# Performance work log

Hardware: AMD Instinct MI355X
Metric: run time of the kernel (lower is better)

The kernel has to match this reference:

```python
import jax, jax.numpy as jnp
import numpy as np
import math

D_MODEL = 1024
N_HEADS = 16
D_HEAD = 64
D_MLP = 4096
INIT_RANGE = 0.02
VAR_EPS = 1e-05
BATCH = 2
SEQ = 2048


def new_gelu(x):
    c = math.sqrt(2.0 / math.pi)
    return 0.5 * x * (1.0 + jnp.tanh(c * (x + 0.044715 * x ** 3)))


def layer_norm(x, w, b):
    mean = jnp.mean(x, axis=-1, keepdims=True)
    x = x - mean
    var = jnp.mean(x * x, axis=-1, keepdims=True)
    return x / jnp.sqrt(var + VAR_EPS) * w + b


def setup_inputs() -> dict:
    key = jax.random.key(0)
    ks = jax.random.split(key, 12)
    s = INIT_RANGE
    return {
        "resid": jax.random.normal(ks[0], (BATCH, SEQ, D_MODEL), jnp.float32),
        "w_q": s * jax.random.normal(ks[1], (N_HEADS, D_MODEL, D_HEAD), jnp.float32),
        "w_k": s * jax.random.normal(ks[2], (N_HEADS, D_MODEL, D_HEAD), jnp.float32),
        "w_v": s * jax.random.normal(ks[3], (N_HEADS, D_MODEL, D_HEAD), jnp.float32),
        "w_o": s * jax.random.normal(ks[4], (N_HEADS, D_HEAD, D_MODEL), jnp.float32),
        "ln1_w": s * jax.random.normal(ks[5], (D_MODEL,), jnp.float32),
        "ln1_b": jnp.zeros((D_MODEL,), jnp.float32),
        "ln2_w": s * jax.random.normal(ks[6], (D_MODEL,), jnp.float32),
        "ln2_b": jnp.zeros((D_MODEL,), jnp.float32),
        "w_in": s * jax.random.normal(ks[7], (D_MODEL, D_MLP), jnp.float32),
        "b_in": jnp.zeros((D_MLP,), jnp.float32),
        "w_out": s * jax.random.normal(ks[8], (D_MLP, D_MODEL), jnp.float32),
        "b_out": jnp.zeros((D_MODEL,), jnp.float32),
    }


def attention(x, w_q, w_k, w_v, w_o):
    # x: [b, s, d]; weights: [h, d, dh] / [h, dh, d]
    qs = jnp.einsum('bsd,hde->bhse', x, w_q)
    ks = jnp.einsum('bsd,hde->bhse', x, w_k)
    vs = jnp.einsum('bsd,hde->bhse', x, w_v)
    attn = jnp.einsum('bhqe,bhke->bhqk', qs, ks)  # [b, h, s, s]
    s = attn.shape[-1]
    causal = jnp.triu(jnp.ones((s, s), dtype=bool), k=1)
    attn = jnp.where(causal, -jnp.inf, attn)
    attn = jax.nn.softmax(attn / math.sqrt(D_HEAD), axis=-1)
    z = jnp.einsum('bhqk,bhke->bhqe', attn, vs)
    return jnp.einsum('bhse,hed->bsd', z, w_o)


def reference(resid, w_q, w_k, w_v, w_o, ln1_w, ln1_b, ln2_w, ln2_b, w_in, b_in, w_out, b_out):
    resid = resid + attention(layer_norm(resid, ln1_w, ln1_b), w_q, w_k, w_v, w_o)
    h = layer_norm(resid, ln2_w, ln2_b)
    h = new_gelu(jnp.einsum('bsd,dm->bsm', h, w_in) + b_in)
    resid = resid + jnp.einsum('bsm,md->bsd', h, w_out) + b_out
    return resid
```

## Files before the change

### kernel.cpp

```cpp
#include <hip/hip_runtime.h>

#define DEV static __device__ __forceinline__

typedef unsigned short u16;
typedef __attribute__((ext_vector_type(8))) __bf16 bf16x8;
typedef __attribute__((ext_vector_type(4))) float f32x4;

DEV float bf2f(u16 u) { union { unsigned int i; float f; } v; v.i = ((unsigned int)u) << 16; return v.f; }
DEV u16 f2bf(float f) {
  union { float f; unsigned int i; } v; v.f = f;
  unsigned int r = v.i + 0x7fffu + ((v.i >> 16) & 1u);
  return (u16)(r >> 16);
}

DEV float gelu_f(float x) {
  float u = 0.7978845608028654f * (x + 0.044715f * x * x * x);
  float e = __expf(2.f * u);
  float t = 1.f - 2.f / (e + 1.f);
  return 0.5f * x * (1.f + t);
}

DEV void async16(const u16* g, u16* l) {
  __builtin_amdgcn_global_load_lds(
      (const __attribute__((address_space(1))) unsigned int*)g,
      (__attribute__((address_space(3))) unsigned int*)l, 16, 0, 0);
}

__global__ __launch_bounds__(256) void transpose_all(
    const float* __restrict__ w_q, const float* __restrict__ w_k,
    const float* __restrict__ w_v, const float* __restrict__ w_o,
    const float* __restrict__ w_in, const float* __restrict__ w_out,
    u16* __restrict__ WQKVT, u16* __restrict__ WOT,
    u16* __restrict__ WINT, u16* __restrict__ WOUTT)
{
  int t = blockIdx.x;
  const float* src; u16* dst; int R, C, c0, r0;
  if (t < 3072) {
    int seg = t >> 10, tt = t & 1023;
    int z = tt >> 6, rem = tt & 63;
    const float* w = seg == 0 ? w_q : (seg == 1 ? w_k : w_v);
    src = w + z * 65536;
    dst = WQKVT + seg * 1048576 + z * 65536;
    R = 1024; C = 64;
    c0 = (rem >> 5) * 32; r0 = (rem & 31) * 32;
  } else if (t < 4096) {
    int tt = t - 3072;
    src = w_o; dst = WOT; R = 1024; C = 1024;
    c0 = (tt & 31) * 32; r0 = (tt >> 5) * 32;
  } else if (t < 8192) {
    int tt = t - 4096;
    src = w_in; dst = WINT; R = 1024; C = 4096;
    c0 = (tt & 127) * 32; r0 = (tt >> 7) * 32;
  } else {
    int tt = t - 8192;
    src = w_out; dst = WOUTT; R = 4096; C = 1024;
    c0 = (tt & 31) * 32; r0 = (tt >> 5) * 32;
  }
  __shared__ float tile[32][33];
  int tx = threadIdx.x & 31, ty = threadIdx.x >> 5;
#pragma unroll
  for (int i = 0; i < 32; i += 8)
    tile[ty + i][tx] = src[(size_t)(r0 + ty + i) * C + (c0 + tx)];
  __syncthreads();
#pragma unroll
  for (int i = 0; i < 32; i += 8)
    dst[(size_t)(c0 + ty + i) * R + (r0 + tx)] = f2bf(tile[tx][ty + i]);
}

__global__ __launch_bounds__(256) void ln_kernel(
    const float* __restrict__ x, const float* __restrict__ g,
    const float* __restrict__ b, u16* __restrict__ out)
{
  int row = blockIdx.x, tid = threadIdx.x;
  const float4 v = ((const float4*)(x + (size_t)row * 1024))[tid];
  float s = v.x + v.y + v.z + v.w;
  float ss = v.x * v.x + v.y * v.y + v.z * v.z + v.w * v.w;
#pragma unroll
  for (int m = 1; m < 64; m <<= 1) { s += __shfl_xor(s, m, 64); ss += __shfl_xor(ss, m, 64); }
  __shared__ float red[8];
  if ((tid & 63) == 0) { red[tid >> 6] = s; red[4 + (tid >> 6)] = ss; }
  __syncthreads();
  s = red[0] + red[1] + red[2] + red[3];
  ss = red[4] + red[5] + red[6] + red[7];
  float mean = s * (1.f / 1024.f);
  float var = ss * (1.f / 1024.f) - mean * mean;
  float rstd = rsqrtf(var + 1e-5f);
  float4 gv = ((const float4*)g)[tid];
  float4 bv = ((const float4*)b)[tid];
  u16* o = out + (size_t)row * 1024 + tid * 4;
  o[0] = f2bf((v.x - mean) * rstd * gv.x + bv.x);
  o[1] = f2bf((v.y - mean) * rstd * gv.y + bv.y);
  o[2] = f2bf((v.z - mean) * rstd * gv.z + bv.z);
  o[3] = f2bf((v.w - mean) * rstd * gv.w + bv.w);
}

template <int EPI, int BM, int BN>
__global__ __launch_bounds__(256) void gemm_bf16(
    const u16* __restrict__ A, const u16* __restrict__ Bt, int K, int N,
    const float* __restrict__ addv, const float* __restrict__ bias,
    float* __restrict__ outF, u16* __restrict__ o0, u16* __restrict__ o1,
    u16* __restrict__ o2)
{
  constexpr int IM = BM / 32, IN = BN / 32;
  __shared__ u16 lA[BM * 64];
  __shared__ u16 lB[BN * 64];
  const int tid = threadIdx.x;
  const int lane = tid & 63, wave = tid >> 6;
  const int wm = wave >> 1, wn = wave & 1;
  const int quad = lane >> 4, l16 = lane & 15;
  const int m0 = blockIdx.y * BM, n0 = blockIdx.x * BN;

  f32x4 acc[IM][IN] = {};

  const int srow = lane >> 3;
  const int soff = ((lane & 7) ^ srow) << 3;

  for (int kt = 0; kt < K; kt += 64) {
    __syncthreads();
#pragma unroll
    for (int q = 0; q < BM / 32; ++q) {
      int rbase = wave * (BM / 4) + q * 8;
      async16(A + (size_t)(m0 + rbase + srow) * K + kt + soff, lA + rbase * 64);
    }
#pragma unroll
    for (int q = 0; q < BN / 32; ++q) {
      int rbase = wave * (BN / 4) + q * 8;
      async16(Bt + (size_t)(n0 + rbase + srow) * K + kt + soff, lB + rbase * 64);
    }
    __syncthreads();
#pragma unroll
    for (int kk = 0; kk < 2; ++kk) {
      bf16x8 af[IM], bfr[IN];
#pragma unroll
      for (int i = 0; i < IM; ++i) {
        int ar = wm * (BM / 2) + i * 16 + l16;
        af[i] = *(const bf16x8*)&lA[ar * 64 + ((((kk * 4) + quad) ^ (ar & 7)) << 3)];
      }
#pragma unroll
      for (int j = 0; j < IN; ++j) {
        int br = wn * (BN / 2) + j * 16 + l16;
        bfr[j] = *(const bf16x8*)&lB[br * 64 + ((((kk * 4) + quad) ^ (br & 7)) << 3)];
      }
#pragma unroll
      for (int i = 0; i < IM; ++i)
#pragma unroll
        for (int j = 0; j < IN; ++j)
          acc[i][j] = __builtin_amdgcn_mfma_f32_16x16x32_bf16(af[i], bfr[j], acc[i][j], 0, 0, 0);
    }
  }

#pragma unroll
  for (int i = 0; i < IM; ++i) {
    const int rowb = m0 + wm * (BM / 2) + i * 16 + quad * 4;
#pragma unroll
    for (int j = 0; j < IN; ++j) {
      const int col = n0 + wn * (BN / 2) + j * 16 + l16;
#pragma unroll
      for (int rr = 0; rr < 4; ++rr) {
        const int m = rowb + rr;
        const float v = acc[i][j][rr];
        if (EPI == 0) {
          int bb = m >> 11, s = m & 2047;
          int proj = col >> 10, hc = col & 1023, hh = hc >> 6, e = hc & 63;
          size_t bhh = (size_t)(bb * 16 + hh);
          if (proj == 0) o0[(bhh * 2048 + s) * 64 + e] = f2bf(v * 0.125f);
          else if (proj == 1) o1[(bhh * 2048 + s) * 64 + e] = f2bf(v);
          else o2[bhh * 131072 + (size_t)e * 2048 + s] = f2bf(v);
        } else if (EPI == 1) {
          size_t idx = (size_t)m * N + col;
          outF[idx] = v + addv[idx];
        } else if (EPI == 2) {
          o0[(size_t)m * N + col] = f2bf(gelu_f(v + bias[col]));
        } else {
          size_t idx = (size_t)m * N + col;
          outF[idx] = v + bias[col] + addv[idx];
        }
      }
    }
  }
}

__global__ __launch_bounds__(256) void attn_flash(
    const u16* __restrict__ Q, const u16* __restrict__ K,
    const u16* __restrict__ Vt, u16* __restrict__ Z)
{
  __shared__ u16 lK[64 * 64];
  __shared__ u16 lV[64 * 64];
  __shared__ u16 lP[4][16 * 64];

  const int tid = threadIdx.x;
  const int lane = tid & 63, wave = tid >> 6;
  const int quad = lane >> 4, l16 = lane & 15;

  const int flat = blockIdx.x;
  const int xcd = flat & 7, w = flat >> 3;
  const int bhid = xcd * 4 + (w >> 5);
  const int qtile = 31 - (w & 31);
  const int b = bhid >> 4, h = bhid & 15;
  const size_t bh = (size_t)bhid;
  const int q0b = qtile * 64;
  const int q0w = q0b + wave * 16;

  const int srow = lane >> 3;
  const int soff = ((lane & 7) ^ srow) << 3;

  bf16x8 qf[2];
#pragma unroll
  for (int d = 0; d < 2; ++d)
    qf[d] = *(const bf16x8*)(Q + (bh * 2048 + (size_t)(q0w + l16)) * 64 + d * 32 + quad * 8);

  f32x4 oacc[4] = {};
  float lrow[4] = {};

  u16* myP = lP[wave];
  const int kend = q0b + 64;

  for (int kt0 = 0; kt0 < kend; kt0 += 64) {
    __syncthreads();
#pragma unroll
    for (int q = 0; q < 2; ++q) {
      int rbase = wave * 16 + q * 8;
      async16(K + (bh * 2048 + (size_t)(kt0 + rbase + srow)) * 64 + soff, lK + rbase * 64);
      async16(Vt + bh * 131072 + (size_t)(rbase + srow) * 2048 + kt0 + soff, lV + rbase * 64);
    }
    __syncthreads();

    bf16x8 kf[4][2];
#pragma unroll
    for (int j = 0; j < 4; ++j)
#pragma unroll
      for (int d = 0; d < 2; ++d) {
        int key = j * 16 + l16;
        kf[j][d] = *(const bf16x8*)(lK + key * 64 + (((d * 4 + quad) ^ (key & 7)) << 3));
      }
    f32x4 sv[4];
#pragma unroll
    for (int j = 0; j < 4; ++j) {
      f32x4 z = {};
      z = __builtin_amdgcn_mfma_f32_16x16x32_bf16(qf[0], kf[j][0], z, 0, 0, 0);
      z = __builtin_amdgcn_mfma_f32_16x16x32_bf16(qf[1], kf[j][1], z, 0, 0, 0);
      sv[j] = z;
    }

    const bool needMask = (kt0 + 63 > q0w);
#pragma unroll
    for (int rr = 0; rr < 4; ++rr) {
      int rowl = quad * 4 + rr;
      int rowg = q0w + rowl;
      u16* prow = myP + rowl * 64;
      float accl = lrow[rr];
#pragma unroll
      for (int j = 0; j < 4; ++j) {
        float p = __expf(sv[j][rr]);
        if (needMask && (kt0 + j * 16 + l16 > rowg)) p = 0.f;
        accl += p;
        int chk = j * 2 + (l16 >> 3);
        prow[((chk ^ (rowl & 7)) << 3) + (l16 & 7)] = (u16)(__float_as_uint(p) >> 16);
      }
      lrow[rr] = accl;
    }

#pragma unroll
    for (int ks = 0; ks < 2; ++ks) {
      int chk = ks * 4 + quad;
      bf16x8 pf, vf[4];
      pf = *(const bf16x8*)(myP + l16 * 64 + ((chk ^ (l16 & 7)) << 3));
#pragma unroll
      for (int d = 0; d < 4; ++d) {
        int dh = d * 16 + l16;
        vf[d] = *(const bf16x8*)(lV + dh * 64 + ((chk ^ (dh & 7)) << 3));
      }
#pragma unroll
      for (int d = 0; d < 4; ++d)
        oacc[d] = __builtin_amdgcn_mfma_f32_16x16x32_bf16(pf, vf[d], oacc[d], 0, 0, 0);
    }
  }

#pragma unroll
  for (int rr = 0; rr < 4; ++rr) {
    float l = lrow[rr];
#pragma unroll
    for (int msk = 1; msk < 16; msk <<= 1) l += __shfl_xor(l, msk, 64);
    lrow[rr] = 1.f / l;
  }
#pragma unroll
  for (int d = 0; d < 4; ++d)
#pragma unroll
    for (int rr = 0; rr < 4; ++rr) {
      int srowq = q0w + quad * 4 + rr;
      Z[((size_t)(b * 2048 + srowq)) * 1024 + h * 64 + d * 16 + l16] =
          f2bf(oacc[d][rr] * lrow[rr]);
    }
}

extern "C" void kernel_launch(void* const* d_in, const int* in_sizes, int n_in,
                              void* d_out, int out_size, void* d_ws, size_t ws_size,
                              hipStream_t stream) {
  const float* resid = (const float*)d_in[0];
  const float* w_q  = (const float*)d_in[1];
  const float* w_k  = (const float*)d_in[2];
  const float* w_v  = (const float*)d_in[3];
  const float* w_o  = (const float*)d_in[4];
  const float* ln1w = (const float*)d_in[5];
  const float* ln1b = (const float*)d_in[6];
  const float* ln2w = (const float*)d_in[7];
  const float* ln2b = (const float*)d_in[8];
  const float* w_in = (const float*)d_in[9];
  const float* b_in = (const float*)d_in[10];
  const float* w_out= (const float*)d_in[11];
  const float* b_out= (const float*)d_in[12];
  float* out = (float*)d_out;

  const size_t MB = 1u << 20;
  char* ws = (char*)d_ws;
  u16* WQKVT = (u16*)(ws + 0);
  u16* WOT   = (u16*)(ws + 6 * MB);
  u16* WINT  = (u16*)(ws + 8 * MB);
  u16* WOUTT = (u16*)(ws + 16 * MB);
  u16* X1    = (u16*)(ws + 24 * MB);
  u16* Qb    = (u16*)(ws + 32 * MB);
  u16* Kb    = (u16*)(ws + 40 * MB);
  u16* Vb    = (u16*)(ws + 48 * MB);
  u16* Zb    = (u16*)(ws + 56 * MB);
  float* R2  = (float*)(ws + 64 * MB);
  u16* Hb    = (u16*)(ws + 80 * MB);
  u16* Gb    = (u16*)(ws + 24 * MB);

  transpose_all<<<dim3(12288), 256, 0, stream>>>(w_q, w_k, w_v, w_o, w_in, w_out,
                                                 WQKVT, WOT, WINT, WOUTT);
  ln_kernel<<<4096, 256, 0, stream>>>(resid, ln1w, ln1b, X1);
  gemm_bf16<0, 64, 128><<<dim3(24, 64), 256, 0, stream>>>(X1, WQKVT, 1024, 3072, nullptr, nullptr, nullptr, Qb, Kb, Vb);
  attn_flash<<<dim3(1024), 256, 0, stream>>>(Qb, Kb, Vb, Zb);
  gemm_bf16<1, 64, 64><<<dim3(16, 64), 256, 0, stream>>>(Zb, WOT, 1024, 1024, resid, nullptr, R2, nullptr, nullptr, nullptr);
  ln_kernel<<<4096, 256, 0, stream>>>(R2, ln2w, ln2b, Hb);
  gemm_bf16<2, 64, 128><<<dim3(32, 64), 256, 0, stream>>>(Hb, WINT, 1024, 4096, nullptr, b_in, nullptr, Gb, nullptr, nullptr);
  gemm_bf16<3, 64, 64><<<dim3(16, 64), 256, 0, stream>>>(Gb, WOUTT, 4096, 1024, R2, b_out, out, nullptr, nullptr, nullptr);
}
```

Baseline: 368.1 us.

## Pair causal query tiles per block and double-buffer K/V loads in attention

Each attention block now handles two query tiles, one long and one short (p and 31-p), so every block does the same 33 key-tile iterations and causal work is balanced across half as many blocks. K/V tiles are double-buffered in LDS, and the next tile's async load is issued before computing on the current one, which drops one barrier per iteration. The cost is doubled K/V LDS use, which may lower occupancy, and a longer serial loop per block.

```diff
diff --git a/kernel.cpp b/kernel.cpp
--- a/kernel.cpp
+++ b/kernel.cpp
@@ -184,8 +184,8 @@
     const u16* __restrict__ Q, const u16* __restrict__ K,
     const u16* __restrict__ Vt, u16* __restrict__ Z)
 {
-  __shared__ u16 lK[64 * 64];
-  __shared__ u16 lV[64 * 64];
+  __shared__ u16 lK[2][64 * 64];
+  __shared__ u16 lV[2][64 * 64];
   __shared__ u16 lP[4][16 * 64];
 
   const int tid = threadIdx.x;
@@ -194,36 +194,82 @@
 
   const int flat = blockIdx.x;
   const int xcd = flat & 7, w = flat >> 3;
-  const int bhid = xcd * 4 + (w >> 5);
-  const int qtile = 31 - (w & 31);
+  const int bhid = xcd * 4 + (w >> 4);
+  const int p = w & 15;
   const int b = bhid >> 4, h = bhid & 15;
   const size_t bh = (size_t)bhid;
-  const int q0b = qtile * 64;
-  const int q0w = q0b + wave * 16;
+
+  const int nA = 32 - p;
+  const int q0A = (31 - p) * 64;
+  const int q0B = p * 64;
 
   const int srow = lane >> 3;
   const int soff = ((lane & 7) ^ srow) << 3;
 
+  u16* myP = lP[wave];
+
+  auto stage = [&](int buf, int s) {
+    int kt0 = (s < nA ? s : s - nA) * 64;
+#pragma unroll
+    for (int q = 0; q < 2; ++q) {
+      int rbase = wave * 16 + q * 8;
+      async16(K + (bh * 2048 + (size_t)(kt0 + rbase + srow)) * 64 + soff,
+              lK[buf] + rbase * 64);
+      async16(Vt + bh * 131072 + (size_t)(rbase + srow) * 2048 + kt0 + soff,
+              lV[buf] + rbase * 64);
+    }
+  };
+
+  stage(0, 0);
+
+  f32x4 oacc[4] = {};
+  float lrow[4] = {};
+  int q0w = q0A + wave * 16;
+
   bf16x8 qf[2];
 #pragma unroll
   for (int d = 0; d < 2; ++d)
     qf[d] = *(const bf16x8*)(Q + (bh * 2048 + (size_t)(q0w + l16)) * 64 + d * 32 + quad * 8);
 
-  f32x4 oacc[4] = {};
-  float lrow[4] = {};
-
-  u16* myP = lP[wave];
-  const int kend = q0b + 64;
-
-  for (int kt0 = 0; kt0 < kend; kt0 += 64) {
+  auto writeO = [&]() {
+#pragma unroll
+    for (int rr = 0; rr < 4; ++rr) {
+      float l = lrow[rr];
+#pragma unroll
+      for (int msk = 1; msk < 16; msk <<= 1) l += __shfl_xor(l, msk, 64);
+      lrow[rr] = 1.f / l;
+    }
+#pragma unroll
+    for (int d = 0; d < 4; ++d)
+#pragma unroll
+      for (int rr = 0; rr < 4; ++rr) {
+        int srowq = q0w + quad * 4 + rr;
+        Z[((size_t)(b * 2048 + srowq)) * 1024 + h * 64 + d * 16 + l16] =
+            f2bf(oacc[d][rr] * lrow[rr]);
+      }
+  };
+
+  for (int s = 0; s < 33; ++s) {
+    if (s == nA) {
+      writeO();
+#pragma unroll
+      for (int d = 0; d < 4; ++d)
+#pragma unroll
+        for (int e = 0; e < 4; ++e) oacc[d][e] = 0.f;
+#pragma unroll
+      for (int rr = 0; rr < 4; ++rr) lrow[rr] = 0.f;
+      q0w = q0B + wave * 16;
+#pragma unroll
+      for (int d = 0; d < 2; ++d)
+        qf[d] = *(const bf16x8*)(Q + (bh * 2048 + (size_t)(q0w + l16)) * 64 + d * 32 + quad * 8);
+    }
+
     __syncthreads();
-#pragma unroll
-    for (int q = 0; q < 2; ++q) {
-      int rbase = wave * 16 + q * 8;
-      async16(K + (bh * 2048 + (size_t)(kt0 + rbase + srow)) * 64 + soff, lK + rbase * 64);
-      async16(Vt + bh * 131072 + (size_t)(rbase + srow) * 2048 + kt0 + soff, lV + rbase * 64);
-    }
-    __syncthreads();
+    if (s < 32) stage((s + 1) & 1, s + 1);
+
+    const u16* cK = lK[s & 1];
+    const u16* cV = lV[s & 1];
+    const int kt0 = (s < nA ? s : s - nA) * 64;
 
     bf16x8 kf[4][2];
 #pragma unroll
@@ -231,7 +277,7 @@
 #pragma unroll
       for (int d = 0; d < 2; ++d) {
         int key = j * 16 + l16;
-        kf[j][d] = *(const bf16x8*)(lK + key * 64 + (((d * 4 + quad) ^ (key & 7)) << 3));
+        kf[j][d] = *(const bf16x8*)(cK + key * 64 + (((d * 4 + quad) ^ (key & 7)) << 3));
       }
     f32x4 sv[4];
 #pragma unroll
@@ -251,11 +297,11 @@
       float accl = lrow[rr];
 #pragma unroll
       for (int j = 0; j < 4; ++j) {
-        float p = __expf(sv[j][rr]);
-        if (needMask && (kt0 + j * 16 + l16 > rowg)) p = 0.f;
-        accl += p;
+        float pv = __expf(sv[j][rr]);
+        if (needMask && (kt0 + j * 16 + l16 > rowg)) pv = 0.f;
+        accl += pv;
         int chk = j * 2 + (l16 >> 3);
-        prow[((chk ^ (rowl & 7)) << 3) + (l16 & 7)] = (u16)(__float_as_uint(p) >> 16);
+        prow[((chk ^ (rowl & 7)) << 3) + (l16 & 7)] = (u16)(__float_as_uint(pv) >> 16);
       }
       lrow[rr] = accl;
     }
@@ -268,7 +314,7 @@
 #pragma unroll
       for (int d = 0; d < 4; ++d) {
         int dh = d * 16 + l16;
-        vf[d] = *(const bf16x8*)(lV + dh * 64 + ((chk ^ (dh & 7)) << 3));
+        vf[d] = *(const bf16x8*)(cV + dh * 64 + ((chk ^ (dh & 7)) << 3));
       }
 #pragma unroll
       for (int d = 0; d < 4; ++d)
@@ -276,21 +322,7 @@
     }
   }
 
-#pragma unroll
-  for (int rr = 0; rr < 4; ++rr) {
-    float l = lrow[rr];
-#pragma unroll
-    for (int msk = 1; msk < 16; msk <<= 1) l += __shfl_xor(l, msk, 64);
-    lrow[rr] = 1.f / l;
-  }
-#pragma unroll
-  for (int d = 0; d < 4; ++d)
-#pragma unroll
-    for (int rr = 0; rr < 4; ++rr) {
-      int srowq = q0w + quad * 4 + rr;
-      Z[((size_t)(b * 2048 + srowq)) * 1024 + h * 64 + d * 16 + l16] =
-          f2bf(oacc[d][rr] * lrow[rr]);
-    }
+  writeO();
 }
 
 extern "C" void kernel_launch(void* const* d_in, const int* in_sizes, int n_in,
@@ -330,7 +362,7 @@
                                                  WQKVT, WOT, WINT, WOUTT);
   ln_kernel<<<4096, 256, 0, stream>>>(resid, ln1w, ln1b, X1);
   gemm_bf16<0, 64, 128><<<dim3(24, 64), 256, 0, stream>>>(X1, WQKVT, 1024, 3072, nullptr, nullptr, nullptr, Qb, Kb, Vb);
-  attn_flash<<<dim3(1024), 256, 0, stream>>>(Qb, Kb, Vb, Zb);
+  attn_flash<<<dim3(512), 256, 0, stream>>>(Qb, Kb, Vb, Zb);
   gemm_bf16<1, 64, 64><<<dim3(16, 64), 256, 0, stream>>>(Zb, WOT, 1024, 1024, resid, nullptr, R2, nullptr, nullptr, nullptr);
   ln_kernel<<<4096, 256, 0, stream>>>(R2, ln2w, ln2b, Hb);
   gemm_bf16<2, 64, 128><<<dim3(32, 64), 256, 0, stream>>>(Hb, WINT, 1024, 4096, nullptr, b_in, nullptr, Gb, nullptr, nullptr);
```

Measured after the change: 359.0 us. 1.03x faster.
